# Optimization experiments

Hardware: AMD Instinct MI355X
Metric: run time of the kernel (lower is better)

The kernel has to match this reference:

```python
import jax, jax.numpy as jnp
import numpy as np

B, S, H = 128, 512, 1024


def setup_inputs() -> dict:
    key = jax.random.key(0)
    ks = jax.random.split(key, 7)
    sc = 1.0 / np.sqrt(H)
    return {
        "emb": jax.random.normal(ks[0], (B, S, H), dtype=jnp.float32),
        "Ww": jax.random.normal(ks[1], (H, H), dtype=jnp.float32) * sc,
        "Wb": jax.random.normal(ks[2], (H,), dtype=jnp.float32) * sc,
        "Uw": jax.random.normal(ks[3], (H, H), dtype=jnp.float32) * sc,
        "Ub": jax.random.normal(ks[4], (H,), dtype=jnp.float32) * sc,
        "Vw": jax.random.normal(ks[5], (H, H), dtype=jnp.float32) * sc,
        "Vb": jax.random.normal(ks[6], (H,), dtype=jnp.float32) * sc,
    }


def reference(emb, Ww, Wb, Uw, Ub, Vw, Vb):
    # torch Linear: y = x @ W.T + b
    def step(p, xi):  # p: [B,H], xi: [B,H]
        p_xi = xi + p
        r = jax.nn.sigmoid(p_xi @ Ww.T + Wb)
        h = jnp.tanh((r * p + xi) @ Vw.T + Vb)
        z = jax.nn.sigmoid(p_xi @ Uw.T + Ub)
        p_new = (1.0 - z) * p + z * h
        return p_new, p_new

    p0 = jnp.zeros((emb.shape[0], emb.shape[2]), dtype=emb.dtype)
    xs = jnp.swapaxes(emb, 0, 1)  # [S,B,H]
    _, ys = jax.lax.scan(step, p0, xs)
    return jnp.swapaxes(ys, 0, 1)  # [B,S,H]
```

## Files before the change

### kernel.cpp

```cpp
#include <hip/hip_runtime.h>
#include <hip/hip_bf16.h>


#define Ss 512
#define Hh 1024
#define NWG 256
#define NTHR 512

typedef __bf16 bf16x8 __attribute__((ext_vector_type(8)));
typedef float f32x4 __attribute__((ext_vector_type(4)));
typedef int   i32x4 __attribute__((ext_vector_type(4)));

__device__ __forceinline__ float sigmoid_fast(float x) { return 1.0f / (1.0f + __expf(-x)); }
__device__ __forceinline__ float tanh_fast(float x) { return 2.0f / (1.0f + __expf(-2.0f * x)) - 1.0f; }

__device__ __forceinline__ void ic_store_bf16(__bf16* p, float v) {
    unsigned u = (unsigned)__builtin_bit_cast(unsigned short, (__bf16)v);
    asm volatile("global_store_short %0, %1, off sc0 sc1" :: "v"(p), "v"(u) : "memory");
}

__device__ __forceinline__ void stage16rows(const char* g, char* stbuf, int tid) {
    int c0 = tid, c1 = tid + 512, c2 = tid + 1024, c3 = tid + 1536;
    const void* a0 = g + (c0 >> 7) * 2048 + (c0 & 127) * 16;
    const void* a1 = g + (c1 >> 7) * 2048 + (c1 & 127) * 16;
    const void* a2 = g + (c2 >> 7) * 2048 + (c2 & 127) * 16;
    const void* a3 = g + (c3 >> 7) * 2048 + (c3 & 127) * 16;
    i32x4 r0, r1, r2, r3;
    asm volatile(
        "global_load_dwordx4 %0, %4, off sc0 sc1\n\t"
        "global_load_dwordx4 %1, %5, off sc0 sc1\n\t"
        "global_load_dwordx4 %2, %6, off sc0 sc1\n\t"
        "global_load_dwordx4 %3, %7, off sc0 sc1\n\t"
        "s_waitcnt vmcnt(0)"
        : "=&v"(r0), "=&v"(r1), "=&v"(r2), "=&v"(r3)
        : "v"(a0), "v"(a1), "v"(a2), "v"(a3));
    *(i32x4*)(stbuf + (c0 >> 7) * 2048 + (((c0 & 127) * 16) ^ (((c0 >> 7) & 7) << 4))) = r0;
    *(i32x4*)(stbuf + (c1 >> 7) * 2048 + (((c1 & 127) * 16) ^ (((c1 >> 7) & 7) << 4))) = r1;
    *(i32x4*)(stbuf + (c2 >> 7) * 2048 + (((c2 & 127) * 16) ^ (((c2 >> 7) & 7) << 4))) = r2;
    *(i32x4*)(stbuf + (c3 >> 7) * 2048 + (((c3 & 127) * 16) ^ (((c3 >> 7) & 7) << 4))) = r3;
}

__device__ __forceinline__ bf16x8 frag(const char* stbuf, int row, int kelem) {
    return *(const bf16x8*)(stbuf + row * 2048 + ((kelem * 2) ^ ((row & 7) << 4)));
}

__device__ __forceinline__ void gbar(unsigned* slots, unsigned ph, int tid, int lw) {
    asm volatile("s_waitcnt vmcnt(0)" ::: "memory");
    __syncthreads();
    if (tid == 0)
        __hip_atomic_store(&slots[lw * 16], ph, __ATOMIC_RELAXED, __HIP_MEMORY_SCOPE_SYSTEM);
    if (tid < 64) {
        for (;;) {
            unsigned v = __hip_atomic_load(&slots[(tid & 31) * 16], __ATOMIC_RELAXED,
                                           __HIP_MEMORY_SCOPE_SYSTEM);
            if (__all((int)(v >= ph))) break;
            __builtin_amdgcn_s_sleep(2);
        }
    }
    __syncthreads();
}

__global__ __launch_bounds__(NTHR, 2) void gru_ic(
    const float* __restrict__ emb, const float* __restrict__ Ww,
    const float* __restrict__ Wb, const float* __restrict__ Uw,
    const float* __restrict__ Ub, const float* __restrict__ Vw,
    const float* __restrict__ Vb,
    __bf16* __restrict__ pxi, __bf16* __restrict__ av,
    unsigned* __restrict__ arr, float* __restrict__ out)
{
    __shared__ char  stbuf[32768];
    __shared__ f32x4 sc[6][64];
    __shared__ float p_lds[16][32];

    const int tid   = threadIdx.x;
    const int lane  = tid & 63;
    const int wid   = tid >> 6;
    const int la    = lane & 15;
    const int lb    = lane >> 4;
    const int wg    = blockIdx.x;
    const int g     = wg & 7;
    const int lw    = wg >> 3;
    const int rbase = g * 16;
    const int n0    = lw * 32;
    const int nt    = wid & 1;
    const int kh    = (wid >> 1) & 1;
    const int kq    = wid >> 1;
    const int jc    = n0 + nt * 16 + la;
    unsigned* slots = arr + g * 512;

    const float* WA = (wid < 4) ? Ww : Uw;
    bf16x8 Wa[16];
#pragma unroll
    for (int i = 0; i < 16; ++i) {
        const float* s = WA + (size_t)jc * Hh + kh * 512 + i * 32 + lb * 8;
        bf16x8 v;
#pragma unroll
        for (int j = 0; j < 8; ++j) v[j] = (__bf16)s[j];
        Wa[i] = v;
    }
    bf16x8 Vf[8];
#pragma unroll
    for (int i = 0; i < 8; ++i) {
        const float* s = Vw + (size_t)jc * Hh + kq * 256 + i * 32 + lb * 8;
        bf16x8 v;
#pragma unroll
        for (int j = 0; j < 8; ++j) v[j] = (__bf16)s[j];
        Vf[i] = v;
    }
    const float bias1 = (wid < 4) ? Wb[jc] : Ub[jc];
    const float bias2 = Vb[jc];

    ((float*)p_lds)[tid] = 0.0f;
    f32x4 pregs = {0.f, 0.f, 0.f, 0.f};
    if (wid == 4 || wid == 5) {
#pragma unroll
        for (int r = 0; r < 4; ++r) {
            int row = rbase + lb * 4 + r;
            ic_store_bf16(pxi + row * Hh + jc, emb[(size_t)row * (Ss * Hh) + jc]);
        }
    }
    unsigned ph = 1;
    gbar(slots, ph, tid, lw);

    const char* pxiG = (const char*)(pxi + (size_t)rbase * Hh);
    const char* avG  = (const char*)(av  + (size_t)rbase * Hh);

    for (int t = 0; t < Ss; ++t) {
        f32x4 embc = {0.f,0.f,0.f,0.f}, embn = embc, zz = embc;
        if (wid == 0 || wid == 1) {
#pragma unroll
            for (int r = 0; r < 4; ++r)
                embc[r] = emb[((size_t)(rbase + lb * 4 + r) * Ss + t) * Hh + jc];
        } else if ((wid == 4 || wid == 5) && t + 1 < Ss) {
#pragma unroll
            for (int r = 0; r < 4; ++r)
                embn[r] = emb[((size_t)(rbase + lb * 4 + r) * Ss + (t + 1)) * Hh + jc];
        }

        stage16rows(pxiG, stbuf, tid);
        __syncthreads();
        f32x4 acc0 = {0.f,0.f,0.f,0.f}, acc1 = acc0;
#pragma unroll
        for (int i = 0; i < 8; ++i) {
            bf16x8 a0 = frag(stbuf, la, kh * 512 + (2 * i) * 32 + lb * 8);
            bf16x8 a1 = frag(stbuf, la, kh * 512 + (2 * i + 1) * 32 + lb * 8);
            acc0 = __builtin_amdgcn_mfma_f32_16x16x32_bf16(a0, Wa[2 * i],     acc0, 0, 0, 0);
            acc1 = __builtin_amdgcn_mfma_f32_16x16x32_bf16(a1, Wa[2 * i + 1], acc1, 0, 0, 0);
        }
        f32x4 acc = acc0 + acc1;
        if (kh == 1) sc[(wid < 4 ? 0 : 2) + nt][lane] = acc;
        __syncthreads();
        if (wid == 0 || wid == 1) {
            acc += sc[nt][lane];
#pragma unroll
            for (int r = 0; r < 4; ++r) {
                int row = rbase + lb * 4 + r;
                float rg = sigmoid_fast(acc[r] + bias1);
                float pc = p_lds[lb * 4 + r][nt * 16 + la];
                ic_store_bf16(av + row * Hh + jc, rg * pc + embc[r]);
            }
        } else if (wid == 4 || wid == 5) {
            acc += sc[2 + nt][lane];
#pragma unroll
            for (int r = 0; r < 4; ++r) zz[r] = sigmoid_fast(acc[r] + bias1);
        }
        gbar(slots, ++ph, tid, lw);

        stage16rows(avG, stbuf, tid);
        __syncthreads();
        f32x4 h0 = {0.f,0.f,0.f,0.f}, h1 = h0;
#pragma unroll
        for (int i = 0; i < 4; ++i) {
            bf16x8 a0 = frag(stbuf, la, kq * 256 + (2 * i) * 32 + lb * 8);
            bf16x8 a1 = frag(stbuf, la, kq * 256 + (2 * i + 1) * 32 + lb * 8);
            h0 = __builtin_amdgcn_mfma_f32_16x16x32_bf16(a0, Vf[2 * i],     h0, 0, 0, 0);
            h1 = __builtin_amdgcn_mfma_f32_16x16x32_bf16(a1, Vf[2 * i + 1], h1, 0, 0, 0);
        }
        f32x4 hacc = h0 + h1;
        if (wid != 4 && wid != 5)
            sc[nt * 3 + (kq == 0 ? 0 : (kq == 1 ? 1 : 2))][lane] = hacc;
        __syncthreads();
        if (wid == 4 || wid == 5) {
            int base = nt * 3;
            hacc += sc[base][lane] + sc[base + 1][lane] + sc[base + 2][lane];
#pragma unroll
            for (int r = 0; r < 4; ++r) {
                int row  = rbase + lb * 4 + r;
                float h  = tanh_fast(hacc[r] + bias2);
                float pn = (1.0f - zz[r]) * pregs[r] + zz[r] * h;
                pregs[r] = pn;
                p_lds[lb * 4 + r][nt * 16 + la] = pn;
                out[((size_t)row * Ss + t) * Hh + jc] = pn;
                if (t + 1 < Ss)
                    ic_store_bf16(pxi + row * Hh + jc, pn + embn[r]);
            }
        }
        if (t + 1 < Ss) gbar(slots, ++ph, tid, lw);
    }
}


extern "C" void kernel_launch(void* const* d_in, const int* in_sizes, int n_in,
                              void* d_out, int out_size, void* d_ws, size_t ws_size,
                              hipStream_t stream) {
    const float* emb = (const float*)d_in[0];
    const float* Ww  = (const float*)d_in[1];
    const float* Wb  = (const float*)d_in[2];
    const float* Uw  = (const float*)d_in[3];
    const float* Ub  = (const float*)d_in[4];
    const float* Vw  = (const float*)d_in[5];
    const float* Vb  = (const float*)d_in[6];
    float* out = (float*)d_out;

    char* ws = (char*)d_ws;
    __bf16*   pxi = (__bf16*)(ws);
    __bf16*   av  = (__bf16*)(ws + 256 * 1024);
    unsigned* arr = (unsigned*)(ws + 512 * 1024);

    hipMemsetAsync(arr, 0, 16384, stream);

    void* args[] = {(void*)&emb, (void*)&Ww, (void*)&Wb, (void*)&Uw, (void*)&Ub,
                    (void*)&Vw, (void*)&Vb, (void*)&pxi, (void*)&av,
                    (void*)&arr, (void*)&out};
    hipError_t e = hipLaunchCooperativeKernel(
        reinterpret_cast<const void*>(gru_ic), dim3(NWG), dim3(NTHR),
        args, 0, stream);
    if (e != hipSuccess) {
        gru_ic<<<dim3(NWG), dim3(NTHR), 0, stream>>>(
            emb, Ww, Wb, Uw, Ub, Vw, Vb, pxi, av, arr, out);
    }
}
```

Baseline: 3.063 ms.

## Replace per-slot group barrier with atomic counter arrive/poll and defer global loads/stores

Replaces the per-workgroup-slot flag barrier with a single atomic counter per row group. Each workgroup does a fetch-add to arrive, and all threads poll the counter with a cache-bypassing load until it reaches the phase target. The out stores and the next step's emb loads move past the arrive point, so they overlap the wait instead of sitting on the critical path. Every thread now spins on the same global address, which may add contention at the shared cache line. The polling loop also drops the previous sleep instruction.

```diff
diff --git a/kernel.cpp b/kernel.cpp
--- a/kernel.cpp
+++ b/kernel.cpp
@@ -17,6 +17,12 @@
 __device__ __forceinline__ void ic_store_bf16(__bf16* p, float v) {
     unsigned u = (unsigned)__builtin_bit_cast(unsigned short, (__bf16)v);
     asm volatile("global_store_short %0, %1, off sc0 sc1" :: "v"(p), "v"(u) : "memory");
+}
+__device__ __forceinline__ unsigned ic_load_u32(const unsigned* p) {
+    unsigned v;
+    asm volatile("global_load_dword %0, %1, off sc0 sc1\n\ts_waitcnt vmcnt(0)"
+                 : "=v"(v) : "v"(p) : "memory");
+    return v;
 }
 
 __device__ __forceinline__ void stage16rows(const char* g, char* stbuf, int tid) {
@@ -44,23 +50,17 @@
     return *(const bf16x8*)(stbuf + row * 2048 + ((kelem * 2) ^ ((row & 7) << 4)));
 }
 
-__device__ __forceinline__ void gbar(unsigned* slots, unsigned ph, int tid, int lw) {
+__device__ __forceinline__ void arrive(unsigned* cnt, int tid) {
     asm volatile("s_waitcnt vmcnt(0)" ::: "memory");
     __syncthreads();
     if (tid == 0)
-        __hip_atomic_store(&slots[lw * 16], ph, __ATOMIC_RELAXED, __HIP_MEMORY_SCOPE_SYSTEM);
-    if (tid < 64) {
-        for (;;) {
-            unsigned v = __hip_atomic_load(&slots[(tid & 31) * 16], __ATOMIC_RELAXED,
-                                           __HIP_MEMORY_SCOPE_SYSTEM);
-            if (__all((int)(v >= ph))) break;
-            __builtin_amdgcn_s_sleep(2);
-        }
-    }
-    __syncthreads();
-}
-
-__global__ __launch_bounds__(NTHR, 2) void gru_ic(
+        (void)__hip_atomic_fetch_add(cnt, 1u, __ATOMIC_RELAXED, __HIP_MEMORY_SCOPE_SYSTEM);
+}
+__device__ __forceinline__ void pollwait(const unsigned* cnt, unsigned target) {
+    while (ic_load_u32(cnt) < target) { }
+}
+
+__global__ __launch_bounds__(NTHR, 2) void gru_v6(
     const float* __restrict__ emb, const float* __restrict__ Ww,
     const float* __restrict__ Wb, const float* __restrict__ Uw,
     const float* __restrict__ Ub, const float* __restrict__ Vw,
@@ -86,7 +86,7 @@
     const int kh    = (wid >> 1) & 1;
     const int kq    = wid >> 1;
     const int jc    = n0 + nt * 16 + la;
-    unsigned* slots = arr + g * 512;
+    unsigned* cnt   = arr + g * 64;
 
     const float* WA = (wid < 4) ? Ww : Uw;
     bf16x8 Wa[16];
@@ -119,27 +119,23 @@
             ic_store_bf16(pxi + row * Hh + jc, emb[(size_t)row * (Ss * Hh) + jc]);
         }
     }
+    f32x4 embc = {0.f, 0.f, 0.f, 0.f};
+    if (wid == 0 || wid == 1) {
+#pragma unroll
+        for (int r = 0; r < 4; ++r)
+            embc[r] = emb[((size_t)(rbase + lb * 4 + r) * Ss + 0) * Hh + jc];
+    }
     unsigned ph = 1;
-    gbar(slots, ph, tid, lw);
+    arrive(cnt, tid);
 
     const char* pxiG = (const char*)(pxi + (size_t)rbase * Hh);
     const char* avG  = (const char*)(av  + (size_t)rbase * Hh);
 
     for (int t = 0; t < Ss; ++t) {
-        f32x4 embc = {0.f,0.f,0.f,0.f}, embn = embc, zz = embc;
-        if (wid == 0 || wid == 1) {
-#pragma unroll
-            for (int r = 0; r < 4; ++r)
-                embc[r] = emb[((size_t)(rbase + lb * 4 + r) * Ss + t) * Hh + jc];
-        } else if ((wid == 4 || wid == 5) && t + 1 < Ss) {
-#pragma unroll
-            for (int r = 0; r < 4; ++r)
-                embn[r] = emb[((size_t)(rbase + lb * 4 + r) * Ss + (t + 1)) * Hh + jc];
-        }
-
+        pollwait(cnt, ph * 32u);
         stage16rows(pxiG, stbuf, tid);
         __syncthreads();
-        f32x4 acc0 = {0.f,0.f,0.f,0.f}, acc1 = acc0;
+        f32x4 acc0 = {0.f, 0.f, 0.f, 0.f}, acc1 = acc0;
 #pragma unroll
         for (int i = 0; i < 8; ++i) {
             bf16x8 a0 = frag(stbuf, la, kh * 512 + (2 * i) * 32 + lb * 8);
@@ -150,6 +146,7 @@
         f32x4 acc = acc0 + acc1;
         if (kh == 1) sc[(wid < 4 ? 0 : 2) + nt][lane] = acc;
         __syncthreads();
+        f32x4 zz = {0.f, 0.f, 0.f, 0.f};
         if (wid == 0 || wid == 1) {
             acc += sc[nt][lane];
 #pragma unroll
@@ -164,11 +161,19 @@
 #pragma unroll
             for (int r = 0; r < 4; ++r) zz[r] = sigmoid_fast(acc[r] + bias1);
         }
-        gbar(slots, ++ph, tid, lw);
-
+        arrive(cnt, tid); ++ph;
+
+        f32x4 embn = {0.f, 0.f, 0.f, 0.f};
+        if ((wid == 4 || wid == 5) && t + 1 < Ss) {
+#pragma unroll
+            for (int r = 0; r < 4; ++r)
+                embn[r] = emb[((size_t)(rbase + lb * 4 + r) * Ss + (t + 1)) * Hh + jc];
+        }
+
+        pollwait(cnt, ph * 32u);
         stage16rows(avG, stbuf, tid);
         __syncthreads();
-        f32x4 h0 = {0.f,0.f,0.f,0.f}, h1 = h0;
+        f32x4 h0 = {0.f, 0.f, 0.f, 0.f}, h1 = h0;
 #pragma unroll
         for (int i = 0; i < 4; ++i) {
             bf16x8 a0 = frag(stbuf, la, kq * 256 + (2 * i) * 32 + lb * 8);
@@ -180,6 +185,7 @@
         if (wid != 4 && wid != 5)
             sc[nt * 3 + (kq == 0 ? 0 : (kq == 1 ? 1 : 2))][lane] = hacc;
         __syncthreads();
+        f32x4 pn = {0.f, 0.f, 0.f, 0.f};
         if (wid == 4 || wid == 5) {
             int base = nt * 3;
             hacc += sc[base][lane] + sc[base + 1][lane] + sc[base + 2][lane];
@@ -187,15 +193,25 @@
             for (int r = 0; r < 4; ++r) {
                 int row  = rbase + lb * 4 + r;
                 float h  = tanh_fast(hacc[r] + bias2);
-                float pn = (1.0f - zz[r]) * pregs[r] + zz[r] * h;
-                pregs[r] = pn;
-                p_lds[lb * 4 + r][nt * 16 + la] = pn;
-                out[((size_t)row * Ss + t) * Hh + jc] = pn;
+                pn[r] = (1.0f - zz[r]) * pregs[r] + zz[r] * h;
+                pregs[r] = pn[r];
+                p_lds[lb * 4 + r][nt * 16 + la] = pn[r];
                 if (t + 1 < Ss)
-                    ic_store_bf16(pxi + row * Hh + jc, pn + embn[r]);
+                    ic_store_bf16(pxi + row * Hh + jc, pn[r] + embn[r]);
             }
         }
-        if (t + 1 < Ss) gbar(slots, ++ph, tid, lw);
+        if (t + 1 < Ss) { arrive(cnt, tid); ++ph; }
+
+        if (wid == 4 || wid == 5) {
+#pragma unroll
+            for (int r = 0; r < 4; ++r)
+                out[((size_t)(rbase + lb * 4 + r) * Ss + t) * Hh + jc] = pn[r];
+        }
+        if ((wid == 0 || wid == 1) && t + 1 < Ss) {
+#pragma unroll
+            for (int r = 0; r < 4; ++r)
+                embc[r] = emb[((size_t)(rbase + lb * 4 + r) * Ss + (t + 1)) * Hh + jc];
+        }
     }
 }
 
@@ -217,16 +233,16 @@
     __bf16*   av  = (__bf16*)(ws + 256 * 1024);
     unsigned* arr = (unsigned*)(ws + 512 * 1024);
 
-    hipMemsetAsync(arr, 0, 16384, stream);
+    hipMemsetAsync(arr, 0, 4096, stream);
 
     void* args[] = {(void*)&emb, (void*)&Ww, (void*)&Wb, (void*)&Uw, (void*)&Ub,
                     (void*)&Vw, (void*)&Vb, (void*)&pxi, (void*)&av,
                     (void*)&arr, (void*)&out};
     hipError_t e = hipLaunchCooperativeKernel(
-        reinterpret_cast<const void*>(gru_ic), dim3(NWG), dim3(NTHR),
+        reinterpret_cast<const void*>(gru_v6), dim3(NWG), dim3(NTHR),
         args, 0, stream);
     if (e != hipSuccess) {
-        gru_ic<<<dim3(NWG), dim3(NTHR), 0, stream>>>(
+        gru_v6<<<dim3(NWG), dim3(NTHR), 0, stream>>>(
             emb, Ww, Wb, Uw, Ub, Vw, Vb, pxi, av, arr, out);
     }
 }
```

Result: slower. 3.689 ms (+20.4%).

## Replace global barriers with per-chunk flags and a dedicated staging wave

Applied to the files above, without the earlier changes.

Each phase no longer waits on a full group barrier. Every wavefront publishes its own flag slot, and a dedicated producer wave streams K-chunks of pxi and av into double LDS buffers as soon as the producing workgroups signal readiness. Consumer waves run chunked MFMA loops that spin on LDS staged-counters, so staging overlaps with compute. Each wave now holds a full-K weight slice (32 fragments) rather than a split-K half, which removes split-K reductions but raises register use and drops occupancy to one block per CU. Global stores are packed through LDS into dwordx2 writes. Together these add spin-wait complexity and a risk of ordering bugs or livelock.

```diff
diff --git a/kernel.cpp b/kernel.cpp
--- a/kernel.cpp
+++ b/kernel.cpp
@@ -6,6 +6,7 @@
 #define Hh 1024
 #define NWG 256
 #define NTHR 512
+#define LDS_TOTAL 76800
 
 typedef __bf16 bf16x8 __attribute__((ext_vector_type(8)));
 typedef float f32x4 __attribute__((ext_vector_type(4)));
@@ -14,17 +15,24 @@
 __device__ __forceinline__ float sigmoid_fast(float x) { return 1.0f / (1.0f + __expf(-x)); }
 __device__ __forceinline__ float tanh_fast(float x) { return 2.0f / (1.0f + __expf(-2.0f * x)) - 1.0f; }
 
+__device__ __forceinline__ unsigned lds_ld(const unsigned* p) {
+    return __hip_atomic_load(p, __ATOMIC_RELAXED, __HIP_MEMORY_SCOPE_WORKGROUP);
+}
+__device__ __forceinline__ void lds_st(unsigned* p, unsigned v) {
+    __hip_atomic_store(p, v, __ATOMIC_RELAXED, __HIP_MEMORY_SCOPE_WORKGROUP);
+}
 __device__ __forceinline__ void ic_store_bf16(__bf16* p, float v) {
     unsigned u = (unsigned)__builtin_bit_cast(unsigned short, (__bf16)v);
     asm volatile("global_store_short %0, %1, off sc0 sc1" :: "v"(p), "v"(u) : "memory");
 }
 
-__device__ __forceinline__ void stage16rows(const char* g, char* stbuf, int tid) {
-    int c0 = tid, c1 = tid + 512, c2 = tid + 1024, c3 = tid + 1536;
-    const void* a0 = g + (c0 >> 7) * 2048 + (c0 & 127) * 16;
-    const void* a1 = g + (c1 >> 7) * 2048 + (c1 & 127) * 16;
-    const void* a2 = g + (c2 >> 7) * 2048 + (c2 & 127) * 16;
-    const void* a3 = g + (c3 >> 7) * 2048 + (c3 & 127) * 16;
+__device__ __forceinline__ void stage_chunks4(char* buf, const char* gsrc, int c0,
+                                              int row, int pc, int swz) {
+    const char* g = gsrc + row * 2048 + pc * 16;
+    const void* a0 = g + (size_t)(c0 + 0) * 64;
+    const void* a1 = g + (size_t)(c0 + 1) * 64;
+    const void* a2 = g + (size_t)(c0 + 2) * 64;
+    const void* a3 = g + (size_t)(c0 + 3) * 64;
     i32x4 r0, r1, r2, r3;
     asm volatile(
         "global_load_dwordx4 %0, %4, off sc0 sc1\n\t"
@@ -34,33 +42,74 @@
         "s_waitcnt vmcnt(0)"
         : "=&v"(r0), "=&v"(r1), "=&v"(r2), "=&v"(r3)
         : "v"(a0), "v"(a1), "v"(a2), "v"(a3));
-    *(i32x4*)(stbuf + (c0 >> 7) * 2048 + (((c0 & 127) * 16) ^ (((c0 >> 7) & 7) << 4))) = r0;
-    *(i32x4*)(stbuf + (c1 >> 7) * 2048 + (((c1 & 127) * 16) ^ (((c1 >> 7) & 7) << 4))) = r1;
-    *(i32x4*)(stbuf + (c2 >> 7) * 2048 + (((c2 & 127) * 16) ^ (((c2 >> 7) & 7) << 4))) = r2;
-    *(i32x4*)(stbuf + (c3 >> 7) * 2048 + (((c3 & 127) * 16) ^ (((c3 >> 7) & 7) << 4))) = r3;
-}
-
-__device__ __forceinline__ bf16x8 frag(const char* stbuf, int row, int kelem) {
-    return *(const bf16x8*)(stbuf + row * 2048 + ((kelem * 2) ^ ((row & 7) << 4)));
-}
-
-__device__ __forceinline__ void gbar(unsigned* slots, unsigned ph, int tid, int lw) {
-    asm volatile("s_waitcnt vmcnt(0)" ::: "memory");
-    __syncthreads();
-    if (tid == 0)
-        __hip_atomic_store(&slots[lw * 16], ph, __ATOMIC_RELAXED, __HIP_MEMORY_SCOPE_SYSTEM);
-    if (tid < 64) {
-        for (;;) {
-            unsigned v = __hip_atomic_load(&slots[(tid & 31) * 16], __ATOMIC_RELAXED,
-                                           __HIP_MEMORY_SCOPE_SYSTEM);
-            if (__all((int)(v >= ph))) break;
-            __builtin_amdgcn_s_sleep(2);
-        }
-    }
-    __syncthreads();
-}
-
-__global__ __launch_bounds__(NTHR, 2) void gru_ic(
+    char* d = buf + row * 64 + swz;
+    *(i32x4*)(d + (c0 + 0) * 1024) = r0;
+    *(i32x4*)(d + (c0 + 1) * 1024) = r1;
+    *(i32x4*)(d + (c0 + 2) * 1024) = r2;
+    *(i32x4*)(d + (c0 + 3) * 1024) = r3;
+}
+__device__ __forceinline__ void stage_chunks1(char* buf, const char* gsrc, int c,
+                                              int row, int pc, int swz) {
+    const void* a = gsrc + row * 2048 + (size_t)c * 64 + pc * 16;
+    i32x4 r;
+    asm volatile("global_load_dwordx4 %0, %1, off sc0 sc1\n\ts_waitcnt vmcnt(0)"
+                 : "=&v"(r) : "v"(a));
+    *(i32x4*)(buf + c * 1024 + row * 64 + swz) = r;
+}
+
+__device__ __forceinline__ void stage_phase(char* buf, const char* gsrc, unsigned* slots,
+                                            unsigned slotTarget, unsigned* stagedCnt,
+                                            unsigned base, unsigned* doneCnt,
+                                            unsigned doneTarget, int lane) {
+    while (lds_ld(doneCnt) < doneTarget) { }
+    const int row = lane >> 2, pc = lane & 3;
+    const int swz = ((pc + (row >> 1)) & 3) << 4;
+    int staged = 0;
+    while (staged < 32) {
+        unsigned v = __hip_atomic_load(&slots[lane * 16], __ATOMIC_RELAXED,
+                                       __HIP_MEMORY_SCOPE_SYSTEM);
+        unsigned long long m = __ballot((int)(v >= slotTarget));
+        unsigned long long pr = m & (m >> 1) & 0x5555555555555555ull;
+        unsigned long long miss = (~pr) & 0x5555555555555555ull;
+        int p = miss ? (int)(__builtin_ctzll(miss) >> 1) : 32;
+        if (p > staged) {
+            while (staged + 4 <= p) { stage_chunks4(buf, gsrc, staged, row, pc, swz); staged += 4; }
+            while (staged < p)      { stage_chunks1(buf, gsrc, staged, row, pc, swz); staged += 1; }
+            asm volatile("s_waitcnt lgkmcnt(0)" ::: "memory");
+            if (lane == 0) lds_st(stagedCnt, base + (unsigned)staged);
+        }
+    }
+}
+
+__device__ __forceinline__ f32x4 chunk_gemm(const char* buf, const unsigned* stagedCnt,
+                                            unsigned base, const bf16x8 (&W)[32],
+                                            int la, int lb) {
+    const char* fb = buf + la * 64 + (((lb + (la >> 1)) & 3) << 4);
+    f32x4 a0 = {0.f, 0.f, 0.f, 0.f}, a1 = a0;
+    int avail = (int)(lds_ld(stagedCnt) - base);
+#pragma unroll
+    for (int i = 0; i < 32; ++i) {
+        while (avail < i + 1) avail = (int)(lds_ld(stagedCnt) - base);
+        bf16x8 a = *(const bf16x8*)(fb + i * 1024);
+        if (i & 1) a1 = __builtin_amdgcn_mfma_f32_16x16x32_bf16(a, W[i], a1, 0, 0, 0);
+        else       a0 = __builtin_amdgcn_mfma_f32_16x16x32_bf16(a, W[i], a0, 0, 0, 0);
+    }
+    return a0 + a1;
+}
+
+__device__ __forceinline__ void pack_store_tile(__bf16* gdst, __bf16* mypack,
+                                                const f32x4& v, int la, int lb, int lane) {
+#pragma unroll
+    for (int r = 0; r < 4; ++r) mypack[(lb * 4 + r) * 20 + la] = (__bf16)v[r];
+    asm volatile("s_waitcnt lgkmcnt(0)" ::: "memory");
+    __builtin_amdgcn_sched_barrier(0);
+    int row = lane >> 2, cg = lane & 3;
+    unsigned long long d = *(const unsigned long long*)(&mypack[row * 20 + cg * 4]);
+    __bf16* dst = gdst + row * Hh + cg * 4;
+    asm volatile("global_store_dwordx2 %0, %1, off sc0 sc1" :: "v"(dst), "v"(d) : "memory");
+}
+
+__global__ __launch_bounds__(NTHR, 1) void gru_v7(
     const float* __restrict__ emb, const float* __restrict__ Ww,
     const float* __restrict__ Wb, const float* __restrict__ Uw,
     const float* __restrict__ Ub, const float* __restrict__ Vw,
@@ -68,134 +117,132 @@
     __bf16* __restrict__ pxi, __bf16* __restrict__ av,
     unsigned* __restrict__ arr, float* __restrict__ out)
 {
-    __shared__ char  stbuf[32768];
-    __shared__ f32x4 sc[6][64];
-    __shared__ float p_lds[16][32];
-
-    const int tid   = threadIdx.x;
-    const int lane  = tid & 63;
-    const int wid   = tid >> 6;
-    const int la    = lane & 15;
-    const int lb    = lane >> 4;
-    const int wg    = blockIdx.x;
-    const int g     = wg & 7;
-    const int lw    = wg >> 3;
-    const int rbase = g * 16;
-    const int n0    = lw * 32;
-    const int nt    = wid & 1;
-    const int kh    = (wid >> 1) & 1;
-    const int kq    = wid >> 1;
-    const int jc    = n0 + nt * 16 + la;
-    unsigned* slots = arr + g * 512;
-
-    const float* WA = (wid < 4) ? Ww : Uw;
-    bf16x8 Wa[16];
-#pragma unroll
-    for (int i = 0; i < 16; ++i) {
-        const float* s = WA + (size_t)jc * Hh + kh * 512 + i * 32 + lb * 8;
-        bf16x8 v;
-#pragma unroll
-        for (int j = 0; j < 8; ++j) v[j] = (__bf16)s[j];
-        Wa[i] = v;
-    }
-    bf16x8 Vf[8];
-#pragma unroll
-    for (int i = 0; i < 8; ++i) {
-        const float* s = Vw + (size_t)jc * Hh + kq * 256 + i * 32 + lb * 8;
-        bf16x8 v;
-#pragma unroll
-        for (int j = 0; j < 8; ++j) v[j] = (__bf16)s[j];
-        Vf[i] = v;
-    }
-    const float bias1 = (wid < 4) ? Wb[jc] : Ub[jc];
-    const float bias2 = Vb[jc];
-
-    ((float*)p_lds)[tid] = 0.0f;
+    extern __shared__ char lds[];
+    char* bufA   = lds;
+    char* bufB   = lds + 32768;
+    float* p_lds = (float*)(lds + 70656);
+    f32x4* sc    = (f32x4*)(lds + 72704);
+    unsigned* ctr = (unsigned*)(lds + 74752);
+    unsigned* stagedA = ctr + 0;
+    unsigned* stagedB = ctr + 16;
+    unsigned* doneA   = ctr + 32;
+    unsigned* doneB   = ctr + 48;
+    unsigned* hcnt    = ctr + 64;
+
+    const int tid = threadIdx.x, lane = tid & 63, wid = tid >> 6;
+    const int la = lane & 15, lb = lane >> 4;
+    const int wg = blockIdx.x, g = wg & 7, lw = wg >> 3;
+    const int rbase = g * 16, n0 = lw * 32, nt = wid & 1;
+    const int jc = n0 + nt * 16 + la;
+    unsigned* slots  = arr + g * 1024;
+    unsigned* myslot = slots + (2 * lw + nt) * 16;
+    __bf16* mypack = (__bf16*)(lds + 65536) + wid * 320;
+
+    const float* wsrc = (wid < 2) ? Ww : ((wid < 4) ? Vw : Uw);
+    bf16x8 Wf[32];
+    if (wid < 6) {
+#pragma unroll
+        for (int i = 0; i < 32; ++i) {
+            const float* s = wsrc + (size_t)jc * Hh + i * 32 + lb * 8;
+            bf16x8 vv;
+#pragma unroll
+            for (int j = 0; j < 8; ++j) vv[j] = (__bf16)s[j];
+            Wf[i] = vv;
+        }
+    }
+    const float b1 = (wid < 2) ? Wb[jc] : ((wid < 4) ? Vb[jc] : Ub[jc]);
+    const float b2 = Vb[jc];
+
+    if (tid < 96) ctr[tid] = 0;
+    p_lds[tid] = 0.f;
     f32x4 pregs = {0.f, 0.f, 0.f, 0.f};
     if (wid == 4 || wid == 5) {
 #pragma unroll
         for (int r = 0; r < 4; ++r) {
             int row = rbase + lb * 4 + r;
-            ic_store_bf16(pxi + row * Hh + jc, emb[(size_t)row * (Ss * Hh) + jc]);
-        }
-    }
-    unsigned ph = 1;
-    gbar(slots, ph, tid, lw);
+            ic_store_bf16(pxi + (size_t)row * Hh + jc, emb[(size_t)row * (Ss * Hh) + jc]);
+        }
+        asm volatile("s_waitcnt vmcnt(0)" ::: "memory");
+        if (lane == 0)
+            __hip_atomic_store(myslot, 1u, __ATOMIC_RELAXED, __HIP_MEMORY_SCOPE_SYSTEM);
+    }
+    __syncthreads();
 
     const char* pxiG = (const char*)(pxi + (size_t)rbase * Hh);
     const char* avG  = (const char*)(av  + (size_t)rbase * Hh);
 
-    for (int t = 0; t < Ss; ++t) {
-        f32x4 embc = {0.f,0.f,0.f,0.f}, embn = embc, zz = embc;
-        if (wid == 0 || wid == 1) {
+    if (wid == 7) {
+        for (int t = 0; t < Ss; ++t) {
+            stage_phase(bufA, pxiG, slots, (unsigned)(2 * t + 1), stagedA,
+                        (unsigned)(32 * t), doneA, (unsigned)(4 * t), lane);
+            stage_phase(bufB, avG,  slots, (unsigned)(2 * t + 2), stagedB,
+                        (unsigned)(32 * t), doneB, (unsigned)(2 * t), lane);
+        }
+    } else if (wid < 2) {
+        __bf16* avdst = av + (size_t)rbase * Hh + n0 + nt * 16;
+        for (int t = 0; t < Ss; ++t) {
+            f32x4 embc;
 #pragma unroll
             for (int r = 0; r < 4; ++r)
                 embc[r] = emb[((size_t)(rbase + lb * 4 + r) * Ss + t) * Hh + jc];
-        } else if ((wid == 4 || wid == 5) && t + 1 < Ss) {
+            f32x4 acc = chunk_gemm(bufA, stagedA, (unsigned)(32 * t), Wf, la, lb);
+            if (lane == 0) atomicAdd(doneA, 1u);
+            f32x4 v4;
+#pragma unroll
+            for (int r = 0; r < 4; ++r) {
+                float rg = sigmoid_fast(acc[r] + b1);
+                float pc = p_lds[(lb * 4 + r) * 32 + nt * 16 + la];
+                v4[r] = rg * pc + embc[r];
+            }
+            pack_store_tile(avdst, mypack, v4, la, lb, lane);
+            asm volatile("s_waitcnt vmcnt(0)" ::: "memory");
+            if (lane == 0)
+                __hip_atomic_store(myslot, (unsigned)(2 * t + 2), __ATOMIC_RELAXED,
+                                   __HIP_MEMORY_SCOPE_SYSTEM);
+        }
+    } else if (wid < 4) {
+        for (int t = 0; t < Ss; ++t) {
+            f32x4 hacc = chunk_gemm(bufB, stagedB, (unsigned)(32 * t), Wf, la, lb);
+            sc[nt * 64 + lane] = hacc;
+            asm volatile("s_waitcnt lgkmcnt(0)" ::: "memory");
+            if (lane == 0) { lds_st(&hcnt[nt * 16], (unsigned)(t + 1)); atomicAdd(doneB, 1u); }
+        }
+    } else if (wid < 6) {
+        __bf16* pxidst = pxi + (size_t)rbase * Hh + n0 + nt * 16;
+        for (int t = 0; t < Ss; ++t) {
+            f32x4 zacc = chunk_gemm(bufA, stagedA, (unsigned)(32 * t), Wf, la, lb);
+            if (lane == 0) atomicAdd(doneA, 1u);
+            f32x4 zz;
+#pragma unroll
+            for (int r = 0; r < 4; ++r) zz[r] = sigmoid_fast(zacc[r] + b1);
+            f32x4 embn = {0.f, 0.f, 0.f, 0.f};
+            if (t + 1 < Ss) {
+#pragma unroll
+                for (int r = 0; r < 4; ++r)
+                    embn[r] = emb[((size_t)(rbase + lb * 4 + r) * Ss + (t + 1)) * Hh + jc];
+            }
+            while (lds_ld(&hcnt[nt * 16]) < (unsigned)(t + 1)) { }
+            f32x4 hacc = sc[nt * 64 + lane];
+            f32x4 pn;
+#pragma unroll
+            for (int r = 0; r < 4; ++r) {
+                float h = tanh_fast(hacc[r] + b2);
+                pn[r] = (1.f - zz[r]) * pregs[r] + zz[r] * h;
+                pregs[r] = pn[r];
+                p_lds[(lb * 4 + r) * 32 + nt * 16 + la] = pn[r];
+            }
+            if (t + 1 < Ss) {
+                f32x4 px = pn + embn;
+                pack_store_tile(pxidst, mypack, px, la, lb, lane);
+                asm volatile("s_waitcnt vmcnt(0)" ::: "memory");
+                if (lane == 0)
+                    __hip_atomic_store(myslot, (unsigned)(2 * t + 3), __ATOMIC_RELAXED,
+                                       __HIP_MEMORY_SCOPE_SYSTEM);
+            }
 #pragma unroll
             for (int r = 0; r < 4; ++r)
-                embn[r] = emb[((size_t)(rbase + lb * 4 + r) * Ss + (t + 1)) * Hh + jc];
-        }
-
-        stage16rows(pxiG, stbuf, tid);
-        __syncthreads();
-        f32x4 acc0 = {0.f,0.f,0.f,0.f}, acc1 = acc0;
-#pragma unroll
-        for (int i = 0; i < 8; ++i) {
-            bf16x8 a0 = frag(stbuf, la, kh * 512 + (2 * i) * 32 + lb * 8);
-            bf16x8 a1 = frag(stbuf, la, kh * 512 + (2 * i + 1) * 32 + lb * 8);
-            acc0 = __builtin_amdgcn_mfma_f32_16x16x32_bf16(a0, Wa[2 * i],     acc0, 0, 0, 0);
-            acc1 = __builtin_amdgcn_mfma_f32_16x16x32_bf16(a1, Wa[2 * i + 1], acc1, 0, 0, 0);
-        }
-        f32x4 acc = acc0 + acc1;
-        if (kh == 1) sc[(wid < 4 ? 0 : 2) + nt][lane] = acc;
-        __syncthreads();
-        if (wid == 0 || wid == 1) {
-            acc += sc[nt][lane];
-#pragma unroll
-            for (int r = 0; r < 4; ++r) {
-                int row = rbase + lb * 4 + r;
-                float rg = sigmoid_fast(acc[r] + bias1);
-                float pc = p_lds[lb * 4 + r][nt * 16 + la];
-                ic_store_bf16(av + row * Hh + jc, rg * pc + embc[r]);
-            }
-        } else if (wid == 4 || wid == 5) {
-            acc += sc[2 + nt][lane];
-#pragma unroll
-            for (int r = 0; r < 4; ++r) zz[r] = sigmoid_fast(acc[r] + bias1);
-        }
-        gbar(slots, ++ph, tid, lw);
-
-        stage16rows(avG, stbuf, tid);
-        __syncthreads();
-        f32x4 h0 = {0.f,0.f,0.f,0.f}, h1 = h0;
-#pragma unroll
-        for (int i = 0; i < 4; ++i) {
-            bf16x8 a0 = frag(stbuf, la, kq * 256 + (2 * i) * 32 + lb * 8);
-            bf16x8 a1 = frag(stbuf, la, kq * 256 + (2 * i + 1) * 32 + lb * 8);
-            h0 = __builtin_amdgcn_mfma_f32_16x16x32_bf16(a0, Vf[2 * i],     h0, 0, 0, 0);
-            h1 = __builtin_amdgcn_mfma_f32_16x16x32_bf16(a1, Vf[2 * i + 1], h1, 0, 0, 0);
-        }
-        f32x4 hacc = h0 + h1;
-        if (wid != 4 && wid != 5)
-            sc[nt * 3 + (kq == 0 ? 0 : (kq == 1 ? 1 : 2))][lane] = hacc;
-        __syncthreads();
-        if (wid == 4 || wid == 5) {
-            int base = nt * 3;
-            hacc += sc[base][lane] + sc[base + 1][lane] + sc[base + 2][lane];
-#pragma unroll
-            for (int r = 0; r < 4; ++r) {
-                int row  = rbase + lb * 4 + r;
-                float h  = tanh_fast(hacc[r] + bias2);
-                float pn = (1.0f - zz[r]) * pregs[r] + zz[r] * h;
-                pregs[r] = pn;
-                p_lds[lb * 4 + r][nt * 16 + la] = pn;
-                out[((size_t)row * Ss + t) * Hh + jc] = pn;
-                if (t + 1 < Ss)
-                    ic_store_bf16(pxi + row * Hh + jc, pn + embn[r]);
-            }
-        }
-        if (t + 1 < Ss) gbar(slots, ++ph, tid, lw);
+                out[((size_t)(rbase + lb * 4 + r) * Ss + t) * Hh + jc] = pn[r];
+        }
     }
 }
 
@@ -217,16 +264,18 @@
     __bf16*   av  = (__bf16*)(ws + 256 * 1024);
     unsigned* arr = (unsigned*)(ws + 512 * 1024);
 
-    hipMemsetAsync(arr, 0, 16384, stream);
+    hipMemsetAsync(arr, 0, 32768, stream);
+    hipFuncSetAttribute(reinterpret_cast<const void*>(gru_v7),
+                        hipFuncAttributeMaxDynamicSharedMemorySize, LDS_TOTAL);
 
     void* args[] = {(void*)&emb, (void*)&Ww, (void*)&Wb, (void*)&Uw, (void*)&Ub,
                     (void*)&Vw, (void*)&Vb, (void*)&pxi, (void*)&av,
                     (void*)&arr, (void*)&out};
     hipError_t e = hipLaunchCooperativeKernel(
-        reinterpret_cast<const void*>(gru_ic), dim3(NWG), dim3(NTHR),
-        args, 0, stream);
+        reinterpret_cast<const void*>(gru_v7), dim3(NWG), dim3(NTHR),
+        args, LDS_TOTAL, stream);
     if (e != hipSuccess) {
-        gru_ic<<<dim3(NWG), dim3(NTHR), 0, stream>>>(
+        gru_v7<<<dim3(NWG), dim3(NTHR), LDS_TOTAL, stream>>>(
             emb, Ww, Wb, Uw, Ub, Vw, Vb, pxi, av, arr, out);
     }
 }
```

Result: slower. 6.673 ms (+117.8%).
